# Optimization experiments

Measured on AMD Instinct MI355X. Metric: run time of the kernel, lower is better.

Reference implementation:

```python
import jax, jax.numpy as jnp
import numpy as np

N_NODES = 200000
N_EDGES = 6400000
N_GRAPHS = 1024
N_EMB = 1032
D = 16


def _gcn_conv(x, W, b, src, dst, n):
    # PyG GCNConv: h = x W; symmetric norm with self-loops; aggregate onto target (dst)
    h = x @ W
    deg = jax.ops.segment_sum(jnp.ones_like(dst, dtype=h.dtype), dst, num_segments=n) + 1.0
    dis = jax.lax.rsqrt(deg)
    norm = dis[src] * dis[dst]                      # [E]
    agg = jax.ops.segment_sum(h[src] * norm[:, None], dst, num_segments=n)
    agg = agg + h * (dis * dis)[:, None]            # self-loop term
    return agg + b


def _protein_embed(ids, edge_index, batch_ids, emb, W1, b1, W2, b2):
    n = ids.shape[0]
    x = emb[ids]                                    # embedding lookup [N, D]
    src, dst = edge_index[0], edge_index[1]
    h = jax.nn.relu(_gcn_conv(x, W1, b1, src, dst, n))
    h = _gcn_conv(h, W2, b2, src, dst, n)
    # global_mean_pool over graphs
    sums = jax.ops.segment_sum(h, batch_ids, num_segments=N_GRAPHS)
    cnt = jax.ops.segment_sum(jnp.ones((n,), h.dtype), batch_ids, num_segments=N_GRAPHS)
    return sums / jnp.maximum(cnt, 1.0)[:, None]    # [B, D]


def setup_inputs() -> dict:
    key = jax.random.key(0)
    ks = jax.random.split(key, 10)
    emb = jax.random.normal(ks[0], (N_EMB, D), jnp.float32) * 0.1
    W1 = jax.random.normal(ks[1], (D, D), jnp.float32) * (1.0 / np.sqrt(D))
    W2 = jax.random.normal(ks[2], (D, D), jnp.float32) * (1.0 / np.sqrt(D))
    fcW = jax.random.normal(ks[3], (6, 2 * D), jnp.float32) * (1.0 / np.sqrt(2 * D))
    b1 = jnp.zeros((D,), jnp.float32)
    b2 = jnp.zeros((D,), jnp.float32)
    fcb = jnp.zeros((6,), jnp.float32)
    rx = jax.random.randint(ks[4], (N_NODES,), 0, N_EMB)
    r_edge_index = jax.random.randint(ks[5], (2, N_EDGES), 0, N_NODES)
    r_batch = jnp.sort(jax.random.randint(ks[6], (N_NODES,), 0, N_GRAPHS))
    lx = jax.random.randint(ks[7], (N_NODES,), 0, N_EMB)
    l_edge_index = jax.random.randint(ks[8], (2, N_EDGES), 0, N_NODES)
    l_batch = jnp.sort(jax.random.randint(ks[9], (N_NODES,), 0, N_GRAPHS))
    return {"emb": emb, "W1": W1, "b1": b1, "W2": W2, "b2": b2, "fcW": fcW, "fcb": fcb,
            "rx": rx, "r_edge_index": r_edge_index, "r_batch": r_batch,
            "lx": lx, "l_edge_index": l_edge_index, "l_batch": l_batch}


def reference(emb, W1, b1, W2, b2, fcW, fcb, rx, r_edge_index, r_batch, lx, l_edge_index, l_batch):
    r = _protein_embed(rx, r_edge_index, r_batch, emb, W1, b1, W2, b2)
    l = _protein_embed(lx, l_edge_index, l_batch, emb, W1, b1, W2, b2)
    h = jnp.concatenate([r, l], axis=1)             # [B, 2D]
    out = h @ fcW.T + fcb                           # [B, 6]
    return out[:, :3], out[:, 3:]
```

## Files before the change

kernel.cpp:

```cpp
#include <hip/hip_runtime.h>
#include <hip/hip_bf16.h>

#define N_NODES 200000
#define N_GRAPHS 1024
#define D 16
#define NEDGE 6400000

#define BNODES 256
#define NBUK 782
#define NCH 640
#define ECHUNK 10000
#define CAP 9216
#define GBLK 12500
#define GHALF 6250

__global__ __launch_bounds__(1024) void pA(
        const int* __restrict__ srcR, const int* __restrict__ dstR,
        const int* __restrict__ srcL, const int* __restrict__ dstL,
        unsigned int* __restrict__ slabR, unsigned int* __restrict__ slabL,
        int* __restrict__ gcurR, int* __restrict__ gcurL) {
    const int* src = blockIdx.y ? srcL : srcR;
    const int* dst = blockIdx.y ? dstL : dstR;
    unsigned int* slab = blockIdx.y ? slabL : slabR;
    int* gcur = blockIdx.y ? gcurL : gcurR;

    __shared__ unsigned int stage[ECHUNK];
    __shared__ unsigned short stageB[ECHUNK];
    __shared__ int lh[NBUK];
    __shared__ int lcur[NBUK];
    __shared__ int wsum[16];
    int t = threadIdx.x;
    int wave = t >> 6, lane = t & 63;
    int base = blockIdx.x * ECHUNK;

    for (int k = t; k < NBUK; k += 1024) lh[k] = 0;
    __syncthreads();
    for (int e = t; e < ECHUNK; e += 1024)
        atomicAdd(&lh[((unsigned int)dst[base + e]) >> 8], 1);
    __syncthreads();

    int v = (t < NBUK) ? lh[t] : 0;
    int x = v;
#pragma unroll
    for (int d0 = 1; d0 < 64; d0 <<= 1) {
        int y = __shfl_up(x, d0, 64);
        if (lane >= d0) x += y;
    }
    if (lane == 63) wsum[wave] = x;
    __syncthreads();
    if (wave == 0 && lane < 16) {
        int s = wsum[lane];
#pragma unroll
        for (int d0 = 1; d0 < 16; d0 <<= 1) {
            int y = __shfl_up(s, d0, 64);
            if (lane >= d0) s += y;
        }
        wsum[lane] = s;
    }
    __syncthreads();
    int excl = x - v + (wave ? wsum[wave - 1] : 0);
    if (t < NBUK) lcur[t] = excl;
    __syncthreads();
    if (t < NBUK) {
        int gb = v ? atomicAdd(&gcur[t], v) : 0;
        lh[t] = gb - excl;
    }
    __syncthreads();

    for (int e = t; e < ECHUNK; e += 1024) {
        int d = dst[base + e];
        int s = src[base + e];
        int buk = ((unsigned int)d) >> 8;
        int pos = atomicAdd(&lcur[buk], 1);
        stage[pos] = ((unsigned int)(d & 255) << 18) | (unsigned int)s;
        stageB[pos] = (unsigned short)buk;
    }
    __syncthreads();
    for (int e = t; e < ECHUNK; e += 1024) {
        int k = stageB[e];
        int off = lh[k] + e;
        slab[(size_t)k * CAP + off] = stage[e];
    }
}

__global__ __launch_bounds__(256) void pB2(
        unsigned int* __restrict__ slabR, unsigned int* __restrict__ slabL,
        const int* __restrict__ gcurR, const int* __restrict__ gcurL,
        int2* __restrict__ metaR, int2* __restrict__ metaL,
        float* __restrict__ disR, float* __restrict__ disL) {
    int y = blockIdx.y;
    unsigned int* slab = y ? slabL : slabR;
    const int* gcur = y ? gcurL : gcurR;
    int2* meta = y ? metaL : metaR;
    float* dis = y ? disL : disR;

    __shared__ unsigned int sin_[CAP];
    __shared__ unsigned int sout[CAP];
    __shared__ int hcnt[BNODES], hoff[BNODES], hcur[BNODES];
    __shared__ int wtot[4];
    int t = threadIdx.x;
    int lane = t & 63, wave = t >> 6;
    int b = blockIdx.x;
    int cnt = gcur[b]; if (cnt > CAP) cnt = CAP;
    unsigned int* sl = slab + (size_t)b * CAP;
    hcnt[t] = 0;
    __syncthreads();

    for (int i = t * 4; i < cnt; i += 1024) {
        uint4 v = *(const uint4*)(sl + i);
        sin_[i] = v.x; sin_[i + 1] = v.y; sin_[i + 2] = v.z; sin_[i + 3] = v.w;
    }
    __syncthreads();

    for (int i = t; i < cnt; i += 256) atomicAdd(&hcnt[sin_[i] >> 18], 1);
    __syncthreads();

    int v2 = hcnt[t];
    int x2 = v2;
#pragma unroll
    for (int d0 = 1; d0 < 64; d0 <<= 1) {
        int yy = __shfl_up(x2, d0, 64);
        if (lane >= d0) x2 += yy;
    }
    if (lane == 63) wtot[wave] = x2;
    __syncthreads();
    int pre2 = 0;
    for (int w2 = 0; w2 < wave; w2++) pre2 += wtot[w2];
    int ex = x2 - v2 + pre2;
    hoff[t] = ex;
    hcur[t] = ex;
    __syncthreads();

    for (int i = t; i < cnt; i += 256) {
        unsigned int r = sin_[i];
        int pp = atomicAdd(&hcur[r >> 18], 1);
        sout[pp] = r & 0x3FFFFu;
    }
    __syncthreads();

    int gb = b * CAP;
    for (int i = t; i < cnt; i += 256) sl[i] = sout[i];
    int node = (b << 8) + t;
    if (node < N_NODES) {
        meta[node] = make_int2(gb + hoff[t], gb + hoff[t] + hcnt[t]);
        dis[node] = rsqrtf((float)hcnt[t] + 1.0f);
    }
}

__global__ __launch_bounds__(256) void t1_kernel(
        const int* __restrict__ idsR, const int* __restrict__ idsL,
        const float* __restrict__ emb, const float* __restrict__ W,
        const float* __restrict__ disR, const float* __restrict__ disL,
        __hip_bfloat16* __restrict__ hsR, __hip_bfloat16* __restrict__ hsL) {
    int y = blockIdx.y;
    const int* ids = y ? idsL : idsR;
    const float* dis = y ? disL : disR;
    __hip_bfloat16* hs = y ? hsL : hsR;
    __shared__ float sW[D][D];
    __shared__ float sx[16][D + 1];
    int t = threadIdx.x;
    int j = t & 15, g = t >> 4;
    sW[g][j] = W[t];
    int i = (blockIdx.x << 4) + g;
    sx[g][j] = emb[(size_t)ids[i] * D + j];
    __syncthreads();
    float acc = 0.f;
#pragma unroll
    for (int k = 0; k < D; k++) acc += sx[g][k] * sW[k][j];
    hs[(size_t)i * D + j] = __float2bfloat16(acc * dis[i]);
}

__global__ __launch_bounds__(256) void g1_kernel(
        const int2* __restrict__ metaR, const int2* __restrict__ metaL,
        const unsigned int* __restrict__ csrR, const unsigned int* __restrict__ csrL,
        const __hip_bfloat16* __restrict__ hs1R, const __hip_bfloat16* __restrict__ hs1L,
        const float* __restrict__ disR, const float* __restrict__ disL,
        const float* __restrict__ b1, const float* __restrict__ W2,
        __hip_bfloat16* __restrict__ hs2R, __hip_bfloat16* __restrict__ hs2L) {
    int half = (blockIdx.x >= GHALF);
    int bx = blockIdx.x - (half ? GHALF : 0);
    const int2* meta = half ? metaL : metaR;
    const unsigned int* csr = half ? csrL : csrR;
    const __hip_bfloat16* hs1 = half ? hs1L : hs1R;
    const float* dis = half ? disL : disR;
    __hip_bfloat16* hs2 = half ? hs2L : hs2R;

    __shared__ float sW[D][D];
    __shared__ float sx[32][D + 1];
    int t = threadIdx.x;
    int jp = t & 7, g = t >> 3;
    sW[t >> 4][t & 15] = W2[t];
    int i = (bx << 5) + g;
    int2 be = meta[i];
    float2 acc = __bfloat1622float2(
        *(const __hip_bfloat162*)(hs1 + (size_t)i * D + 2 * jp));
    int e = be.x, end = be.y;
    for (; e + 8 <= end; e += 8) {
        int my = (int)csr[e + jp];
#pragma unroll
        for (int n = 0; n < 8; n++) {
            int s = __shfl(my, n, 8);
            float2 f = __bfloat1622float2(
                *(const __hip_bfloat162*)(hs1 + (size_t)s * D + 2 * jp));
            acc.x += f.x; acc.y += f.y;
        }
    }
    for (; e < end; e++) {
        int s = csr[e];
        float2 f = __bfloat1622float2(
            *(const __hip_bfloat162*)(hs1 + (size_t)s * D + 2 * jp));
        acc.x += f.x; acc.y += f.y;
    }
    float di = dis[i];
    sx[g][2 * jp]     = fmaxf(acc.x * di + b1[2 * jp], 0.f);
    sx[g][2 * jp + 1] = fmaxf(acc.y * di + b1[2 * jp + 1], 0.f);
    __syncthreads();
    float a0 = 0.f, a1 = 0.f;
#pragma unroll
    for (int k = 0; k < D; k++) {
        float xv = sx[g][k];
        a0 += xv * sW[k][2 * jp];
        a1 += xv * sW[k][2 * jp + 1];
    }
    *(__hip_bfloat162*)(hs2 + (size_t)i * D + 2 * jp) =
        __float22bfloat162_rn(make_float2(a0 * di, a1 * di));
}

__global__ __launch_bounds__(256) void g2_kernel(
        const int2* __restrict__ metaR, const int2* __restrict__ metaL,
        const unsigned int* __restrict__ csrR, const unsigned int* __restrict__ csrL,
        const __hip_bfloat16* __restrict__ hs2R, const __hip_bfloat16* __restrict__ hs2L,
        const float* __restrict__ disR, const float* __restrict__ disL,
        const float* __restrict__ b2,
        const int* __restrict__ batR, const int* __restrict__ batL,
        float* __restrict__ sumsR, float* __restrict__ sumsL,
        float* __restrict__ cntR, float* __restrict__ cntL) {
    int half = (blockIdx.x >= GHALF);
    int bx = blockIdx.x - (half ? GHALF : 0);
    const int2* meta = half ? metaL : metaR;
    const unsigned int* csr = half ? csrL : csrR;
    const __hip_bfloat16* hs2 = half ? hs2L : hs2R;
    const float* dis = half ? disL : disR;
    const int* batch = half ? batL : batR;
    float* sums = half ? sumsL : sumsR;
    float* cnt = half ? cntL : cntR;

    __shared__ float sv[32][D + 1];
    __shared__ int sb[32];
    int t = threadIdx.x;
    int jp = t & 7, g = t >> 3;
    int i = (bx << 5) + g;
    int2 be = meta[i];
    float2 acc = __bfloat1622float2(
        *(const __hip_bfloat162*)(hs2 + (size_t)i * D + 2 * jp));
    int e = be.x, end = be.y;
    for (; e + 8 <= end; e += 8) {
        int my = (int)csr[e + jp];
#pragma unroll
        for (int n = 0; n < 8; n++) {
            int s = __shfl(my, n, 8);
            float2 f = __bfloat1622float2(
                *(const __hip_bfloat162*)(hs2 + (size_t)s * D + 2 * jp));
            acc.x += f.x; acc.y += f.y;
        }
    }
    for (; e < end; e++) {
        int s = csr[e];
        float2 f = __bfloat1622float2(
            *(const __hip_bfloat162*)(hs2 + (size_t)s * D + 2 * jp));
        acc.x += f.x; acc.y += f.y;
    }
    float di = dis[i];
    int bi = batch[i];
    sv[g][2 * jp]     = acc.x * di + b2[2 * jp];
    sv[g][2 * jp + 1] = acc.y * di + b2[2 * jp + 1];
    if (jp == 0) sb[g] = bi;
    __syncthreads();
    bool runend = (g == 31) || (sb[g + 1] != bi);
    if (runend) {
        float s0 = 0.f, s1 = 0.f;
        int gg = g;
        while (gg >= 0 && sb[gg] == bi) { s0 += sv[gg][2 * jp]; s1 += sv[gg][2 * jp + 1]; gg--; }
        atomicAdd(&sums[bi * D + 2 * jp], s0);
        atomicAdd(&sums[bi * D + 2 * jp + 1], s1);
        if (jp == 0) atomicAdd(&cnt[bi], (float)(g - gg));
    }
}

__global__ void final_kernel(const float* __restrict__ rs, const float* __restrict__ rc,
                             const float* __restrict__ ls, const float* __restrict__ lc,
                             const float* __restrict__ fcW, const float* __restrict__ fcb,
                             float* __restrict__ out) {
    int b = blockIdx.x * blockDim.x + threadIdx.x;
    if (b >= N_GRAPHS) return;
    float hc[2 * D];
    float rn = fmaxf(rc[b], 1.f), ln = fmaxf(lc[b], 1.f);
#pragma unroll
    for (int j = 0; j < D; j++) {
        hc[j]     = rs[b * D + j] / rn;
        hc[D + j] = ls[b * D + j] / ln;
    }
#pragma unroll
    for (int c = 0; c < 6; c++) {
        float acc = fcb[c];
#pragma unroll
        for (int j = 0; j < 2 * D; j++) acc += hc[j] * fcW[c * 2 * D + j];
        if (c < 3) out[b * 3 + c] = acc;
        else       out[N_GRAPHS * 3 + b * 3 + (c - 3)] = acc;
    }
}

extern "C" void kernel_launch(void* const* d_in, const int* in_sizes, int n_in,
                              void* d_out, int out_size, void* d_ws, size_t ws_size,
                              hipStream_t stream) {
    const float* emb = (const float*)d_in[0];
    const float* W1  = (const float*)d_in[1];
    const float* b1  = (const float*)d_in[2];
    const float* W2  = (const float*)d_in[3];
    const float* b2  = (const float*)d_in[4];
    const float* fcW = (const float*)d_in[5];
    const float* fcb = (const float*)d_in[6];
    const int* rx = (const int*)d_in[7];
    const int* re = (const int*)d_in[8];
    const int* rb = (const int*)d_in[9];
    const int* lx = (const int*)d_in[10];
    const int* le = (const int*)d_in[11];
    const int* lb = (const int*)d_in[12];
    float* out = (float*)d_out;

    char* w = (char*)d_ws;
    unsigned int* slabR = (unsigned int*)w;    w += (size_t)NBUK * CAP * 4;
    unsigned int* slabL = (unsigned int*)w;    w += (size_t)NBUK * CAP * 4;
    __hip_bfloat16* hs1R = (__hip_bfloat16*)w; w += (size_t)N_NODES * D * 2;
    __hip_bfloat16* hs1L = (__hip_bfloat16*)w; w += (size_t)N_NODES * D * 2;
    __hip_bfloat16* hs2R = (__hip_bfloat16*)w; w += (size_t)N_NODES * D * 2;
    __hip_bfloat16* hs2L = (__hip_bfloat16*)w; w += (size_t)N_NODES * D * 2;
    int2* metaR = (int2*)w;                    w += (size_t)N_NODES * 8;
    int2* metaL = (int2*)w;                    w += (size_t)N_NODES * 8;
    float* disR = (float*)w;                   w += (size_t)N_NODES * 4;
    float* disL = (float*)w;                   w += (size_t)N_NODES * 4;
    char* zbase = w;
    int* gcurR = (int*)w;                      w += (size_t)NBUK * 4;
    int* gcurL = (int*)w;                      w += (size_t)NBUK * 4;
    float* sums0 = (float*)w;                  w += (size_t)N_GRAPHS * D * 4;
    float* cnt0  = (float*)w;                  w += (size_t)N_GRAPHS * 4;
    float* sums1 = (float*)w;                  w += (size_t)N_GRAPHS * D * 4;
    float* cnt1  = (float*)w;                  w += (size_t)N_GRAPHS * 4;
    size_t zsize = (size_t)(w - zbase);

    const int* srcR = re;  const int* dstR = re + NEDGE;
    const int* srcL = le;  const int* dstL = le + NEDGE;

    hipMemsetAsync(zbase, 0, zsize, stream);

    pA<<<dim3(NCH, 2), 1024, 0, stream>>>(srcR, dstR, srcL, dstL,
                                          slabR, slabL, gcurR, gcurL);
    pB2<<<dim3(NBUK, 2), 256, 0, stream>>>(slabR, slabL, gcurR, gcurL,
                                           metaR, metaL, disR, disL);

    t1_kernel<<<dim3(GBLK, 2), 256, 0, stream>>>(rx, lx, emb, W1, disR, disL, hs1R, hs1L);
    g1_kernel<<<2 * GHALF, 256, 0, stream>>>(metaR, metaL, slabR, slabL,
                                             hs1R, hs1L, disR, disL, b1, W2, hs2R, hs2L);
    g2_kernel<<<2 * GHALF, 256, 0, stream>>>(metaR, metaL, slabR, slabL,
                                             hs2R, hs2L, disR, disL, b2, rb, lb,
                                             sums0, sums1, cnt0, cnt1);
    final_kernel<<<(N_GRAPHS + 255) / 256, 256, 0, stream>>>(
        sums0, cnt0, sums1, cnt1, fcW, fcb, out);
}
```

Before: 530.9 us.

## Fuse embedding transform into bucket-sort kernel and drop LDS staging copy

Removes the separate t1 kernel and computes the first-layer x·W1·dis transform inside pB2, two threads per node, each writing 8 bf16 outputs. pB2 now uses 512 threads, reads the slab directly from global memory twice instead of staging it in shared memory, and adds a bounds guard on sout writes. This saves one launch and one round trip of dis through global memory, and halves LDS use so more blocks can be resident. The cost is redundant global reads of the slab and extra register pressure from the fused matmul.

```diff
diff --git a/kernel.cpp b/kernel.cpp
--- a/kernel.cpp
+++ b/kernel.cpp
@@ -11,7 +11,6 @@
 #define NCH 640
 #define ECHUNK 10000
 #define CAP 9216
-#define GBLK 12500
 #define GHALF 6250
 
 __global__ __launch_bounds__(1024) void pA(
@@ -83,91 +82,95 @@
     }
 }
 
-__global__ __launch_bounds__(256) void pB2(
+__global__ __launch_bounds__(512) void pB2(
         unsigned int* __restrict__ slabR, unsigned int* __restrict__ slabL,
         const int* __restrict__ gcurR, const int* __restrict__ gcurL,
+        const int* __restrict__ idsR, const int* __restrict__ idsL,
+        const float* __restrict__ emb, const float* __restrict__ W1,
         int2* __restrict__ metaR, int2* __restrict__ metaL,
-        float* __restrict__ disR, float* __restrict__ disL) {
+        float* __restrict__ disR, float* __restrict__ disL,
+        __hip_bfloat16* __restrict__ hs1R, __hip_bfloat16* __restrict__ hs1L) {
     int y = blockIdx.y;
     unsigned int* slab = y ? slabL : slabR;
     const int* gcur = y ? gcurL : gcurR;
+    const int* ids = y ? idsL : idsR;
     int2* meta = y ? metaL : metaR;
     float* dis = y ? disL : disR;
-
-    __shared__ unsigned int sin_[CAP];
+    __hip_bfloat16* hs1 = y ? hs1L : hs1R;
+
     __shared__ unsigned int sout[CAP];
     __shared__ int hcnt[BNODES], hoff[BNODES], hcur[BNODES];
+    __shared__ float sW[D][D];
     __shared__ int wtot[4];
     int t = threadIdx.x;
-    int lane = t & 63, wave = t >> 6;
     int b = blockIdx.x;
+    if (t < 256) { sW[t >> 4][t & 15] = W1[t]; hcnt[t] = 0; }
     int cnt = gcur[b]; if (cnt > CAP) cnt = CAP;
     unsigned int* sl = slab + (size_t)b * CAP;
-    hcnt[t] = 0;
-    __syncthreads();
-
-    for (int i = t * 4; i < cnt; i += 1024) {
-        uint4 v = *(const uint4*)(sl + i);
-        sin_[i] = v.x; sin_[i + 1] = v.y; sin_[i + 2] = v.z; sin_[i + 3] = v.w;
-    }
-    __syncthreads();
-
-    for (int i = t; i < cnt; i += 256) atomicAdd(&hcnt[sin_[i] >> 18], 1);
-    __syncthreads();
-
-    int v2 = hcnt[t];
+    __syncthreads();
+
+    for (int i = t; i < cnt; i += 512)
+        atomicAdd(&hcnt[sl[i] >> 18], 1);
+    __syncthreads();
+
+    int lane = t & 63, wave = t >> 6;
+    int v2 = (t < 256) ? hcnt[t] : 0;
     int x2 = v2;
 #pragma unroll
     for (int d0 = 1; d0 < 64; d0 <<= 1) {
         int yy = __shfl_up(x2, d0, 64);
         if (lane >= d0) x2 += yy;
     }
-    if (lane == 63) wtot[wave] = x2;
-    __syncthreads();
-    int pre2 = 0;
-    for (int w2 = 0; w2 < wave; w2++) pre2 += wtot[w2];
-    int ex = x2 - v2 + pre2;
-    hoff[t] = ex;
-    hcur[t] = ex;
-    __syncthreads();
-
-    for (int i = t; i < cnt; i += 256) {
-        unsigned int r = sin_[i];
+    if (t < 256 && lane == 63) wtot[wave] = x2;
+    __syncthreads();
+    if (t < 256) {
+        int pre2 = 0;
+        for (int w2 = 0; w2 < wave; w2++) pre2 += wtot[w2];
+        int ex = x2 - v2 + pre2;
+        hoff[t] = ex;
+        hcur[t] = ex;
+    }
+    __syncthreads();
+
+    for (int i = t; i < cnt; i += 512) {
+        unsigned int r = sl[i];
         int pp = atomicAdd(&hcur[r >> 18], 1);
-        sout[pp] = r & 0x3FFFFu;
-    }
-    __syncthreads();
-
-    int gb = b * CAP;
-    for (int i = t; i < cnt; i += 256) sl[i] = sout[i];
-    int node = (b << 8) + t;
+        if (pp < CAP) sout[pp] = r & 0x3FFFFu;
+    }
+    __syncthreads();
+
+    for (int i = t; i < cnt; i += 512) sl[i] = sout[i];
+
+    int tt = t >> 1, hf = t & 1;
+    int node = (b << 8) + tt;
     if (node < N_NODES) {
-        meta[node] = make_int2(gb + hoff[t], gb + hoff[t] + hcnt[t]);
-        dis[node] = rsqrtf((float)hcnt[t] + 1.0f);
-    }
-}
-
-__global__ __launch_bounds__(256) void t1_kernel(
-        const int* __restrict__ idsR, const int* __restrict__ idsL,
-        const float* __restrict__ emb, const float* __restrict__ W,
-        const float* __restrict__ disR, const float* __restrict__ disL,
-        __hip_bfloat16* __restrict__ hsR, __hip_bfloat16* __restrict__ hsL) {
-    int y = blockIdx.y;
-    const int* ids = y ? idsL : idsR;
-    const float* dis = y ? disL : disR;
-    __hip_bfloat16* hs = y ? hsL : hsR;
-    __shared__ float sW[D][D];
-    __shared__ float sx[16][D + 1];
-    int t = threadIdx.x;
-    int j = t & 15, g = t >> 4;
-    sW[g][j] = W[t];
-    int i = (blockIdx.x << 4) + g;
-    sx[g][j] = emb[(size_t)ids[i] * D + j];
-    __syncthreads();
-    float acc = 0.f;
-#pragma unroll
-    for (int k = 0; k < D; k++) acc += sx[g][k] * sW[k][j];
-    hs[(size_t)i * D + j] = __float2bfloat16(acc * dis[i]);
+        int hc = hcnt[tt];
+        float di = rsqrtf((float)hc + 1.0f);
+        int gb = b * CAP;
+        if (hf == 0) {
+            meta[node] = make_int2(gb + hoff[tt], gb + hoff[tt] + hc);
+            dis[node] = di;
+        }
+        const float4* er = (const float4*)(emb + (size_t)ids[node] * D);
+        float4 e0 = er[0], e1 = er[1], e2 = er[2], e3 = er[3];
+        float ex_[D] = {e0.x, e0.y, e0.z, e0.w, e1.x, e1.y, e1.z, e1.w,
+                        e2.x, e2.y, e2.z, e2.w, e3.x, e3.y, e3.z, e3.w};
+        int j0 = hf * 8;
+        float o[8];
+#pragma unroll
+        for (int jj = 0; jj < 8; jj++) {
+            float a = 0.f;
+#pragma unroll
+            for (int k = 0; k < D; k++) a += ex_[k] * sW[k][j0 + jj];
+            o[jj] = a * di;
+        }
+        uint4 ov;
+        __hip_bfloat162* q = (__hip_bfloat162*)&ov;
+#pragma unroll
+        for (int jj = 0; jj < 4; jj++)
+            q[jj] = __float22bfloat162_rn(make_float2(o[2 * jj], o[2 * jj + 1]));
+        *(uint4*)(hs1 + (size_t)node * D + j0) = ov;
+    }
 }
 
 __global__ __launch_bounds__(256) void g1_kernel(
@@ -355,10 +358,10 @@
 
     pA<<<dim3(NCH, 2), 1024, 0, stream>>>(srcR, dstR, srcL, dstL,
                                           slabR, slabL, gcurR, gcurL);
-    pB2<<<dim3(NBUK, 2), 256, 0, stream>>>(slabR, slabL, gcurR, gcurL,
-                                           metaR, metaL, disR, disL);
-
-    t1_kernel<<<dim3(GBLK, 2), 256, 0, stream>>>(rx, lx, emb, W1, disR, disL, hs1R, hs1L);
+    pB2<<<dim3(NBUK, 2), 512, 0, stream>>>(slabR, slabL, gcurR, gcurL,
+                                           rx, lx, emb, W1,
+                                           metaR, metaL, disR, disL, hs1R, hs1L);
+
     g1_kernel<<<2 * GHALF, 256, 0, stream>>>(metaR, metaL, slabR, slabL,
                                              hs1R, hs1L, disR, disL, b1, W2, hs2R, hs2L);
     g2_kernel<<<2 * GHALF, 256, 0, stream>>>(metaR, metaL, slabR, slabL,
```

Result: faster. 513.3 us (-3.3%).
